# Kernel optimization log

Hardware: AMD Instinct MI355X
Metric: run time of the kernel (lower is better)

## Reference

```python
import jax, jax.numpy as jnp
import numpy as np

N_NODES = 100000
N_EDGES = 1600000
IN_CH = 64
HID = 64
OUT_CH = 1


def setup_inputs() -> dict:
    key = jax.random.key(0)
    ks = jax.random.split(key, 6)
    x = jax.random.normal(ks[0], (N_NODES, IN_CH), dtype=jnp.float32)
    edge_index = jax.random.randint(ks[1], (2, N_EDGES), 0, N_NODES, dtype=jnp.int64)
    edge_weight = jax.random.uniform(ks[2], (N_EDGES,), dtype=jnp.float32)
    W1 = jax.random.normal(ks[3], (IN_CH, HID), dtype=jnp.float32) / np.sqrt(IN_CH)
    b1 = jnp.zeros((HID,), dtype=jnp.float32)
    W2 = jax.random.normal(ks[4], (HID, OUT_CH), dtype=jnp.float32) / np.sqrt(HID)
    b2 = jnp.zeros((OUT_CH,), dtype=jnp.float32)
    return {"x": x, "edge_index": edge_index, "edge_weight": edge_weight,
            "W1": W1, "b1": b1, "W2": W2, "b2": b2}


def _gcn_conv(x, row, col, ew, W, b, n_nodes):
    # PyG GCNConv: add self-loops (weight 1), symmetric deg normalization,
    # linear (no bias) -> message x_j * norm -> sum at target -> + bias.
    loop = jnp.arange(n_nodes, dtype=row.dtype)
    r = jnp.concatenate([row, loop])
    c = jnp.concatenate([col, loop])
    w = jnp.concatenate([ew, jnp.ones((n_nodes,), dtype=ew.dtype)])
    deg = jax.ops.segment_sum(w, c, num_segments=n_nodes)  # [N]
    dinv = jnp.where(deg > 0, jax.lax.rsqrt(deg), 0.0)
    norm = dinv[r] * w * dinv[c]  # [E+N]
    h = x @ W  # [N, out]
    msg = h[r] * norm[:, None]  # [E+N, out] gather
    out = jax.ops.segment_sum(msg, c, num_segments=n_nodes)  # scatter-add
    return out + b


def reference(x, edge_index, edge_weight, W1, b1, W2, b2):
    row, col = edge_index[0], edge_index[1]
    n = x.shape[0]
    h = _gcn_conv(x, row, col, edge_weight, W1, b1, n)
    h = jax.nn.relu(h)
    out = _gcn_conv(h, row, col, edge_weight, W2, b2, n)
    return out
```

## Files before the change

kernel.cpp:

```cpp
#include <hip/hip_runtime.h>


#define N_NODES 100000
#define N_EDGES 1600000
#define CNT_SHIFT 42
#define SUM_MASK ((1ull << CNT_SHIFT) - 1)
#define BSZ 256
#define NBUCK 391
#define NB1 512
#define EPB 3125

typedef _Float16 half2v __attribute__((ext_vector_type(2)));

__global__ void p1_hist(const int* __restrict__ idx, int* __restrict__ hist) {
    __shared__ int h[NBUCK];
    int t = threadIdx.x, blk = blockIdx.x;
    for (int i = t; i < NBUCK; i += 256) h[i] = 0;
    __syncthreads();
    int e0 = blk * EPB;
    for (int i = t; i < EPB; i += 256) {
        int c = idx[N_EDGES + e0 + i];
        atomicAdd(&h[c >> 8], 1);
    }
    __syncthreads();
    for (int i = t; i < NBUCK; i += 256) hist[(size_t)i * NB1 + blk] = h[i];
}

__global__ void p2a_scan(int* __restrict__ hist, int* __restrict__ btot) {
    __shared__ int s[NB1];
    int t = threadIdx.x, b = blockIdx.x;
    int v = hist[(size_t)b * NB1 + t];
    s[t] = v;
    __syncthreads();
#pragma unroll
    for (int d = 1; d < NB1; d <<= 1) {
        int u = (t >= d) ? s[t - d] : 0;
        __syncthreads();
        s[t] += u;
        __syncthreads();
    }
    hist[(size_t)b * NB1 + t] = s[t] - v;
    if (t == NB1 - 1) btot[b] = s[NB1 - 1];
}

__global__ void p2b_scan(const int* __restrict__ btot, int* __restrict__ boff) {
    __shared__ int s[512];
    int t = threadIdx.x;
    int v = (t < NBUCK) ? btot[t] : 0;
    s[t] = v;
    __syncthreads();
#pragma unroll
    for (int d = 1; d < 512; d <<= 1) {
        int u = (t >= d) ? s[t - d] : 0;
        __syncthreads();
        s[t] += u;
        __syncthreads();
    }
    if (t < NBUCK) boff[t] = s[t] - v;
    if (t == 511) boff[NBUCK] = s[511];
}

__global__ void p3_part(const int* __restrict__ idx, const float* __restrict__ w,
                        const int* __restrict__ hist, const int* __restrict__ boff,
                        float2* __restrict__ bin) {
    __shared__ int h[NBUCK];
    __shared__ int base[NBUCK];
    int t = threadIdx.x, blk = blockIdx.x;
    for (int i = t; i < NBUCK; i += 256) {
        h[i] = 0;
        base[i] = boff[i] + hist[(size_t)i * NB1 + blk];
    }
    __syncthreads();
    int e0 = blk * EPB;
    for (int i = t; i < EPB; i += 256) {
        int e = e0 + i;
        int r = idx[e];
        int c = idx[N_EDGES + e];
        int b = c >> 8;
        int lr = atomicAdd(&h[b], 1);
        bin[base[b] + lr] = make_float2(__int_as_float(r | ((c & 255) << 17)), w[e]);
    }
}

__global__ void p4a_count(const float2* __restrict__ bin, const int* __restrict__ boff,
                          int* __restrict__ cnt, int* __restrict__ off,
                          float* __restrict__ dinv) {
    __shared__ unsigned long long pk[BSZ];
    __shared__ int s[BSZ];
    int t = threadIdx.x, b = blockIdx.x;
    if (t < BSZ) pk[t] = 0ull;
    __syncthreads();
    int s0 = boff[b], s1 = boff[b + 1];
    for (int j = s0 + t; j < s1; j += 512) {
        float2 p = bin[j];
        int cl = (__float_as_int(p.x) >> 17) & 255;
        unsigned long long add =
            (1ull << CNT_SHIFT) | (unsigned long long)(p.y * 4294967296.0f);
        atomicAdd(&pk[cl], add);
    }
    __syncthreads();
    unsigned long long p = 0;
    int c = 0;
    if (t < BSZ) {
        p = pk[t];
        c = (int)(p >> CNT_SHIFT);
        s[t] = c;
    }
    __syncthreads();
#pragma unroll
    for (int d = 1; d < BSZ; d <<= 1) {
        int u = (t >= d && t < BSZ) ? s[t - d] : 0;
        __syncthreads();
        if (t < BSZ) s[t] += u;
        __syncthreads();
    }
    if (t < BSZ) {
        int node = b * BSZ + t;
        if (node < N_NODES) {
            off[node] = s0 + s[t] - c;
            cnt[node] = c;
            float deg = 1.0f + (float)(p & SUM_MASK) * 2.3283064365386963e-10f;
            dinv[node] = rsqrtf(deg);
        }
    }
}

__global__ void p4b_place(const float2* __restrict__ bin, const int* __restrict__ boff,
                          const int* __restrict__ off, const float* __restrict__ dinv,
                          float2* __restrict__ pairs) {
    __shared__ int rk[BSZ];
    int t = threadIdx.x, b = blockIdx.x;
    if (t < BSZ) rk[t] = 0;
    __syncthreads();
    int s0 = boff[b], s1 = boff[b + 1];
    for (int j = s0 + t; j < s1; j += 512) {
        float2 p = bin[j];
        int bits = __float_as_int(p.x);
        int r = bits & 0x1FFFF;
        int cl = (bits >> 17) & 255;
        int c = (b << 8) + cl;
        int rank = atomicAdd(&rk[cl], 1);
        float norm = dinv[r] * p.y * dinv[c];
        pairs[off[c] + rank] = make_float2(__int_as_float(r), norm);
    }
}

__global__ void gemm1(const float* __restrict__ x, const float* __restrict__ W1,
                      _Float16* __restrict__ h1) {
    __shared__ float w1s[64 * 64];
    __shared__ float xs[64 * 64];
    int t = threadIdx.x;
    int row0 = blockIdx.x * 64;

    const float4* W4 = (const float4*)W1;
    float4* w1s4 = (float4*)w1s;
    float4* xs4 = (float4*)xs;
    const float4* X4 = (const float4*)(x + (size_t)row0 * 64);
#pragma unroll
    for (int i = 0; i < 4; i++) {
        w1s4[t + 256 * i] = W4[t + 256 * i];
        int gr = row0 + ((t + 256 * i) >> 4);
        xs4[t + 256 * i] = (gr < N_NODES) ? X4[t + 256 * i]
                                          : make_float4(0.f, 0.f, 0.f, 0.f);
    }
    __syncthreads();

    int cq = t & 15;
    int rq = t >> 4;
    float4 acc0 = {0,0,0,0}, acc1 = {0,0,0,0}, acc2 = {0,0,0,0}, acc3 = {0,0,0,0};
#pragma unroll 4
    for (int k = 0; k < 64; k++) {
        float4 wv = w1s4[k * 16 + cq];
        float x0 = xs[(rq     ) * 64 + k];
        float x1 = xs[(rq + 16) * 64 + k];
        float x2 = xs[(rq + 32) * 64 + k];
        float x3 = xs[(rq + 48) * 64 + k];
        acc0.x += x0*wv.x; acc0.y += x0*wv.y; acc0.z += x0*wv.z; acc0.w += x0*wv.w;
        acc1.x += x1*wv.x; acc1.y += x1*wv.y; acc1.z += x1*wv.z; acc1.w += x1*wv.w;
        acc2.x += x2*wv.x; acc2.y += x2*wv.y; acc2.z += x2*wv.z; acc2.w += x2*wv.w;
        acc3.x += x3*wv.x; acc3.y += x3*wv.y; acc3.z += x3*wv.z; acc3.w += x3*wv.w;
    }
    float4 accs[4] = {acc0, acc1, acc2, acc3};
#pragma unroll
    for (int i = 0; i < 4; i++) {
        int row = row0 + rq + 16 * i;
        if (row < N_NODES) {
            half2v h01 = {(_Float16)accs[i].x, (_Float16)accs[i].y};
            half2v h23 = {(_Float16)accs[i].z, (_Float16)accs[i].w};
            half2v* dst = (half2v*)(h1 + (size_t)row * 64 + 4 * cq);
            dst[0] = h01;
            dst[1] = h23;
        }
    }
}

__global__ void gather1(const half2v* __restrict__ h1v, const float2* __restrict__ pairs,
                        const int* __restrict__ off, const int* __restrict__ cnt,
                        const float* __restrict__ dinv, const float* __restrict__ b1,
                        const float* __restrict__ W2, const float* __restrict__ b2,
                        float* __restrict__ h2, float* __restrict__ out, int n) {
    int t = threadIdx.x;
    int lane = t & 63;
    int half = lane >> 5;
    int cl = lane & 31;
    int dst = blockIdx.x * 2 + (t >> 6);
    if (dst >= n) return;
    int beg = off[dst];
    int end = beg + cnt[dst];
    float di = dinv[dst];
    float a0 = 0.f, a1 = 0.f, b0 = 0.f, b1a = 0.f;
    float c0 = 0.f, c1 = 0.f, d0 = 0.f, d1 = 0.f;
    int j = beg + half;
    for (; j + 14 < end; j += 16) {
        float2 p0 = pairs[j],      p1 = pairs[j + 2],  p2 = pairs[j + 4],  p3 = pairs[j + 6];
        float2 p4 = pairs[j + 8],  p5 = pairs[j + 10], p6 = pairs[j + 12], p7 = pairs[j + 14];
        half2v v0 = h1v[__float_as_int(p0.x) * 32 + cl];
        half2v v1 = h1v[__float_as_int(p1.x) * 32 + cl];
        half2v v2 = h1v[__float_as_int(p2.x) * 32 + cl];
        half2v v3 = h1v[__float_as_int(p3.x) * 32 + cl];
        half2v v4 = h1v[__float_as_int(p4.x) * 32 + cl];
        half2v v5 = h1v[__float_as_int(p5.x) * 32 + cl];
        half2v v6 = h1v[__float_as_int(p6.x) * 32 + cl];
        half2v v7 = h1v[__float_as_int(p7.x) * 32 + cl];
        a0 += p0.y * (float)v0[0]; a1 += p0.y * (float)v0[1];
        b0 += p1.y * (float)v1[0]; b1a += p1.y * (float)v1[1];
        c0 += p2.y * (float)v2[0]; c1 += p2.y * (float)v2[1];
        d0 += p3.y * (float)v3[0]; d1 += p3.y * (float)v3[1];
        a0 += p4.y * (float)v4[0]; a1 += p4.y * (float)v4[1];
        b0 += p5.y * (float)v5[0]; b1a += p5.y * (float)v5[1];
        c0 += p6.y * (float)v6[0]; c1 += p6.y * (float)v6[1];
        d0 += p7.y * (float)v7[0]; d1 += p7.y * (float)v7[1];
    }
    for (; j + 6 < end; j += 8) {
        float2 p0 = pairs[j], p1 = pairs[j + 2], p2 = pairs[j + 4], p3 = pairs[j + 6];
        half2v v0 = h1v[__float_as_int(p0.x) * 32 + cl];
        half2v v1 = h1v[__float_as_int(p1.x) * 32 + cl];
        half2v v2 = h1v[__float_as_int(p2.x) * 32 + cl];
        half2v v3 = h1v[__float_as_int(p3.x) * 32 + cl];
        a0 += p0.y * (float)v0[0]; a1 += p0.y * (float)v0[1];
        b0 += p1.y * (float)v1[0]; b1a += p1.y * (float)v1[1];
        c0 += p2.y * (float)v2[0]; c1 += p2.y * (float)v2[1];
        d0 += p3.y * (float)v3[0]; d1 += p3.y * (float)v3[1];
    }
    for (; j < end; j += 2) {
        float2 p = pairs[j];
        half2v v = h1v[__float_as_int(p.x) * 32 + cl];
        a0 += p.y * (float)v[0]; a1 += p.y * (float)v[1];
    }
    float t0 = (a0 + b0) + (c0 + d0);
    float t1 = (a1 + b1a) + (c1 + d1);
    t0 += __shfl_xor(t0, 32, 64);
    t1 += __shfl_xor(t1, 32, 64);
    half2v sv = h1v[dst * 32 + cl];
    t0 += (float)sv[0] * di * di;
    t1 += (float)sv[1] * di * di;
    float2 b1p = ((const float2*)b1)[cl];
    float v0 = fmaxf(t0 + b1p.x, 0.0f);
    float v1 = fmaxf(t1 + b1p.y, 0.0f);
    float2 w2p = ((const float2*)W2)[cl];
    float p = v0 * w2p.x + v1 * w2p.y;
#pragma unroll
    for (int o = 16; o > 0; o >>= 1) p += __shfl_xor(p, o, 64);
    if (lane == 0) {
        h2[dst] = p;
        out[dst] = b2[0] + p * di * di;
    }
}

__global__ void gather2(const float2* __restrict__ pairs, const int* __restrict__ off,
                        const int* __restrict__ cnt, const float* __restrict__ h2,
                        float* __restrict__ out, int n) {
    int i = blockIdx.x * blockDim.x + threadIdx.x;
    if (i >= n) return;
    int beg = off[i];
    int end = beg + cnt[i];
    float s = 0.f;
#pragma unroll 4
    for (int j = beg; j < end; j++) {
        float2 p = pairs[j];
        s += p.y * h2[__float_as_int(p.x)];
    }
    out[i] += s;
}

extern "C" void kernel_launch(void* const* d_in, const int* in_sizes, int n_in,
                              void* d_out, int out_size, void* d_ws, size_t ws_size,
                              hipStream_t stream) {
    const float* x   = (const float*)d_in[0];
    const int*   idx = (const int*)d_in[1];
    const float* ew  = (const float*)d_in[2];
    const float* W1  = (const float*)d_in[3];
    const float* b1  = (const float*)d_in[4];
    const float* W2  = (const float*)d_in[5];
    const float* b2  = (const float*)d_in[6];
    float* out = (float*)d_out;

    const int N = N_NODES;
    const int E = N_EDGES;

    float* ws = (float*)d_ws;
    int*    off  = (int*)ws;
    int*    cnt  = (int*)(ws + (size_t)N);
    float*  dinv = ws + 2 * (size_t)N;
    int*    boff = (int*)(ws + 3 * (size_t)N);
    int*    btot = (int*)(ws + 3 * (size_t)N + 392);
    int*    hist = (int*)(ws + 300784);
    float2* bin  = (float2*)(ws + 300784 + 200192);
    _Float16* h1 = (_Float16*)(ws + 300784);
    float2* pairs = (float2*)(ws + 3700976);
    float*  h2   = ws + 6900976;

    p1_hist<<<NB1, 256, 0, stream>>>(idx, hist);
    p2a_scan<<<NBUCK, NB1, 0, stream>>>(hist, btot);
    p2b_scan<<<1, 512, 0, stream>>>(btot, boff);
    p3_part<<<NB1, 256, 0, stream>>>(idx, ew, hist, boff, bin);
    p4a_count<<<NBUCK, 512, 0, stream>>>(bin, boff, cnt, off, dinv);
    p4b_place<<<NBUCK, 512, 0, stream>>>(bin, boff, off, dinv, pairs);
    gemm1<<<(N + 63) / 64, 256, 0, stream>>>(x, W1, h1);
    gather1<<<(N + 1) / 2, 128, 0, stream>>>((const half2v*)h1, pairs, off, cnt, dinv,
                                             b1, W2, b2, h2, out, N);
    gather2<<<(N + 255) / 256, 256, 0, stream>>>(pairs, off, cnt, h2, out, N);
}
```

Before: 228.4 us.

## Fuse scan and CSR build kernels, prescale by dinv, retile GEMM, parallelize gather2

Folds the bucket-offset scan into p3_part and p4_build by having each block redundantly rescan btot. Merges the count and place passes into one kernel that keeps offsets and dinv in shared memory, so the per-edge norm needs only the target's dinv. The source-side dinv is folded into h1 and h2 at production time, which removes a gather of dinv[r] per edge. The cnt array is replaced by off[n+1]. gemm1 is retiled to 128 rows with an 8x8 register tile and padded LDS, and gather2 uses 4 lanes per node with shuffle reduction. The cost is redundant scans in every block and higher register pressure in gemm1.

```diff
diff --git a/kernel.cpp b/kernel.cpp
--- a/kernel.cpp
+++ b/kernel.cpp
@@ -43,36 +43,30 @@
     if (t == NB1 - 1) btot[b] = s[NB1 - 1];
 }
 
-__global__ void p2b_scan(const int* __restrict__ btot, int* __restrict__ boff) {
-    __shared__ int s[512];
-    int t = threadIdx.x;
+__global__ void p3_part(const int* __restrict__ idx, const float* __restrict__ w,
+                        const int* __restrict__ hist, const int* __restrict__ btot,
+                        float2* __restrict__ bin) {
+    __shared__ int sc[512];
+    __shared__ int base[NBUCK];
+    __shared__ int h[NBUCK];
+    int t = threadIdx.x, blk = blockIdx.x;
     int v = (t < NBUCK) ? btot[t] : 0;
-    s[t] = v;
+    sc[t] = v;
     __syncthreads();
 #pragma unroll
     for (int d = 1; d < 512; d <<= 1) {
-        int u = (t >= d) ? s[t - d] : 0;
-        __syncthreads();
-        s[t] += u;
-        __syncthreads();
-    }
-    if (t < NBUCK) boff[t] = s[t] - v;
-    if (t == 511) boff[NBUCK] = s[511];
-}
-
-__global__ void p3_part(const int* __restrict__ idx, const float* __restrict__ w,
-                        const int* __restrict__ hist, const int* __restrict__ boff,
-                        float2* __restrict__ bin) {
-    __shared__ int h[NBUCK];
-    __shared__ int base[NBUCK];
-    int t = threadIdx.x, blk = blockIdx.x;
-    for (int i = t; i < NBUCK; i += 256) {
-        h[i] = 0;
-        base[i] = boff[i] + hist[(size_t)i * NB1 + blk];
+        int u = (t >= d) ? sc[t - d] : 0;
+        __syncthreads();
+        sc[t] += u;
+        __syncthreads();
+    }
+    if (t < NBUCK) {
+        base[t] = sc[t] - v + hist[(size_t)t * NB1 + blk];
+        h[t] = 0;
     }
     __syncthreads();
     int e0 = blk * EPB;
-    for (int i = t; i < EPB; i += 256) {
+    for (int i = t; i < EPB; i += 512) {
         int e = e0 + i;
         int r = idx[e];
         int c = idx[N_EDGES + e];
@@ -82,15 +76,28 @@
     }
 }
 
-__global__ void p4a_count(const float2* __restrict__ bin, const int* __restrict__ boff,
-                          int* __restrict__ cnt, int* __restrict__ off,
-                          float* __restrict__ dinv) {
+__global__ void p4_build(const float2* __restrict__ bin, const int* __restrict__ btot,
+                         int* __restrict__ off, float* __restrict__ dinv,
+                         float2* __restrict__ pairs) {
+    __shared__ int sc[512];
     __shared__ unsigned long long pk[BSZ];
-    __shared__ int s[BSZ];
+    __shared__ float dl[BSZ];
+    __shared__ int ofl[BSZ];
+    __shared__ int rk[BSZ];
     int t = threadIdx.x, b = blockIdx.x;
-    if (t < BSZ) pk[t] = 0ull;
-    __syncthreads();
-    int s0 = boff[b], s1 = boff[b + 1];
+    int v = (t < NBUCK) ? btot[t] : 0;
+    sc[t] = v;
+    if (t < BSZ) { pk[t] = 0ull; rk[t] = 0; }
+    __syncthreads();
+#pragma unroll
+    for (int d = 1; d < 512; d <<= 1) {
+        int u = (t >= d) ? sc[t - d] : 0;
+        __syncthreads();
+        sc[t] += u;
+        __syncthreads();
+    }
+    int s0 = (b > 0) ? sc[b - 1] : 0;
+    int s1 = sc[b];
     for (int j = s0 + t; j < s1; j += 512) {
         float2 p = bin[j];
         int cl = (__float_as_int(p.x) >> 17) & 255;
@@ -99,106 +106,121 @@
         atomicAdd(&pk[cl], add);
     }
     __syncthreads();
-    unsigned long long p = 0;
+    unsigned long long pv = 0;
     int c = 0;
     if (t < BSZ) {
-        p = pk[t];
-        c = (int)(p >> CNT_SHIFT);
-        s[t] = c;
+        pv = pk[t];
+        c = (int)(pv >> CNT_SHIFT);
+        sc[t] = c;
     }
     __syncthreads();
 #pragma unroll
     for (int d = 1; d < BSZ; d <<= 1) {
-        int u = (t >= d && t < BSZ) ? s[t - d] : 0;
-        __syncthreads();
-        if (t < BSZ) s[t] += u;
+        int u = (t >= d && t < BSZ) ? sc[t - d] : 0;
+        __syncthreads();
+        if (t < BSZ) sc[t] += u;
         __syncthreads();
     }
     if (t < BSZ) {
+        int o = s0 + sc[t] - c;
+        ofl[t] = o;
+        float deg = 1.0f + (float)(pv & SUM_MASK) * 2.3283064365386963e-10f;
+        float di = rsqrtf(deg);
+        dl[t] = di;
         int node = b * BSZ + t;
-        if (node < N_NODES) {
-            off[node] = s0 + s[t] - c;
-            cnt[node] = c;
-            float deg = 1.0f + (float)(p & SUM_MASK) * 2.3283064365386963e-10f;
-            dinv[node] = rsqrtf(deg);
-        }
-    }
-}
-
-__global__ void p4b_place(const float2* __restrict__ bin, const int* __restrict__ boff,
-                          const int* __restrict__ off, const float* __restrict__ dinv,
-                          float2* __restrict__ pairs) {
-    __shared__ int rk[BSZ];
-    int t = threadIdx.x, b = blockIdx.x;
-    if (t < BSZ) rk[t] = 0;
-    __syncthreads();
-    int s0 = boff[b], s1 = boff[b + 1];
+        if (node < N_NODES) { off[node] = o; dinv[node] = di; }
+    }
+    if (b == NBUCK - 1 && t == 0) off[N_NODES] = s1;
+    __syncthreads();
     for (int j = s0 + t; j < s1; j += 512) {
         float2 p = bin[j];
         int bits = __float_as_int(p.x);
         int r = bits & 0x1FFFF;
         int cl = (bits >> 17) & 255;
-        int c = (b << 8) + cl;
         int rank = atomicAdd(&rk[cl], 1);
-        float norm = dinv[r] * p.y * dinv[c];
-        pairs[off[c] + rank] = make_float2(__int_as_float(r), norm);
+        pairs[ofl[cl] + rank] = make_float2(__int_as_float(r), p.y * dl[cl]);
     }
 }
 
 __global__ void gemm1(const float* __restrict__ x, const float* __restrict__ W1,
-                      _Float16* __restrict__ h1) {
+                      const float* __restrict__ dinv, _Float16* __restrict__ h1) {
+    __shared__ float xs[128 * 68];
     __shared__ float w1s[64 * 64];
-    __shared__ float xs[64 * 64];
     int t = threadIdx.x;
-    int row0 = blockIdx.x * 64;
-
-    const float4* W4 = (const float4*)W1;
+    int row0 = blockIdx.x * 128;
+
+    const float4* W4g = (const float4*)W1;
     float4* w1s4 = (float4*)w1s;
-    float4* xs4 = (float4*)xs;
-    const float4* X4 = (const float4*)(x + (size_t)row0 * 64);
-#pragma unroll
-    for (int i = 0; i < 4; i++) {
-        w1s4[t + 256 * i] = W4[t + 256 * i];
-        int gr = row0 + ((t + 256 * i) >> 4);
-        xs4[t + 256 * i] = (gr < N_NODES) ? X4[t + 256 * i]
-                                          : make_float4(0.f, 0.f, 0.f, 0.f);
-    }
-    __syncthreads();
-
-    int cq = t & 15;
-    int rq = t >> 4;
-    float4 acc0 = {0,0,0,0}, acc1 = {0,0,0,0}, acc2 = {0,0,0,0}, acc3 = {0,0,0,0};
-#pragma unroll 4
-    for (int k = 0; k < 64; k++) {
-        float4 wv = w1s4[k * 16 + cq];
-        float x0 = xs[(rq     ) * 64 + k];
-        float x1 = xs[(rq + 16) * 64 + k];
-        float x2 = xs[(rq + 32) * 64 + k];
-        float x3 = xs[(rq + 48) * 64 + k];
-        acc0.x += x0*wv.x; acc0.y += x0*wv.y; acc0.z += x0*wv.z; acc0.w += x0*wv.w;
-        acc1.x += x1*wv.x; acc1.y += x1*wv.y; acc1.z += x1*wv.z; acc1.w += x1*wv.w;
-        acc2.x += x2*wv.x; acc2.y += x2*wv.y; acc2.z += x2*wv.z; acc2.w += x2*wv.w;
-        acc3.x += x3*wv.x; acc3.y += x3*wv.y; acc3.z += x3*wv.z; acc3.w += x3*wv.w;
-    }
-    float4 accs[4] = {acc0, acc1, acc2, acc3};
-#pragma unroll
-    for (int i = 0; i < 4; i++) {
+#pragma unroll
+    for (int i = 0; i < 8; i++) w1s4[t + 128 * i] = W4g[t + 128 * i];
+    const float4* X4 = (const float4*)x;
+#pragma unroll
+    for (int i = 0; i < 16; i++) {
+        int fi = t + 128 * i;
+        int rl = fi >> 4;
+        int kq = fi & 15;
+        int row = row0 + rl;
+        float4 vv = (row < N_NODES) ? X4[(size_t)row * 16 + kq]
+                                    : make_float4(0.f, 0.f, 0.f, 0.f);
+        *(float4*)&xs[rl * 68 + kq * 4] = vv;
+    }
+    __syncthreads();
+
+    int cq = t & 7;
+    int rq = t >> 3;
+    float acc[8][8];
+#pragma unroll
+    for (int i = 0; i < 8; i++)
+#pragma unroll
+        for (int j = 0; j < 8; j++) acc[i][j] = 0.f;
+
+    for (int k = 0; k < 64; k += 4) {
+        float4 xv[8];
+#pragma unroll
+        for (int i = 0; i < 8; i++)
+            xv[i] = *(const float4*)&xs[(rq + 16 * i) * 68 + k];
+        float4 wv[4][2];
+#pragma unroll
+        for (int kk = 0; kk < 4; kk++) {
+            wv[kk][0] = w1s4[(k + kk) * 16 + 2 * cq];
+            wv[kk][1] = w1s4[(k + kk) * 16 + 2 * cq + 1];
+        }
+#pragma unroll
+        for (int i = 0; i < 8; i++) {
+            float xk[4] = {xv[i].x, xv[i].y, xv[i].z, xv[i].w};
+#pragma unroll
+            for (int kk = 0; kk < 4; kk++) {
+                acc[i][0] += xk[kk] * wv[kk][0].x;
+                acc[i][1] += xk[kk] * wv[kk][0].y;
+                acc[i][2] += xk[kk] * wv[kk][0].z;
+                acc[i][3] += xk[kk] * wv[kk][0].w;
+                acc[i][4] += xk[kk] * wv[kk][1].x;
+                acc[i][5] += xk[kk] * wv[kk][1].y;
+                acc[i][6] += xk[kk] * wv[kk][1].z;
+                acc[i][7] += xk[kk] * wv[kk][1].w;
+            }
+        }
+    }
+#pragma unroll
+    for (int i = 0; i < 8; i++) {
         int row = row0 + rq + 16 * i;
         if (row < N_NODES) {
-            half2v h01 = {(_Float16)accs[i].x, (_Float16)accs[i].y};
-            half2v h23 = {(_Float16)accs[i].z, (_Float16)accs[i].w};
-            half2v* dst = (half2v*)(h1 + (size_t)row * 64 + 4 * cq);
-            dst[0] = h01;
-            dst[1] = h23;
+            float di = dinv[row];
+            half2v h4[4];
+#pragma unroll
+            for (int j = 0; j < 4; j++)
+                h4[j] = half2v{(_Float16)(acc[i][2 * j] * di),
+                               (_Float16)(acc[i][2 * j + 1] * di)};
+            *(float4*)(h1 + (size_t)row * 64 + 8 * cq) = *(float4*)h4;
         }
     }
 }
 
 __global__ void gather1(const half2v* __restrict__ h1v, const float2* __restrict__ pairs,
-                        const int* __restrict__ off, const int* __restrict__ cnt,
-                        const float* __restrict__ dinv, const float* __restrict__ b1,
-                        const float* __restrict__ W2, const float* __restrict__ b2,
-                        float* __restrict__ h2, float* __restrict__ out, int n) {
+                        const int* __restrict__ off, const float* __restrict__ dinv,
+                        const float* __restrict__ b1, const float* __restrict__ W2,
+                        const float* __restrict__ b2, float* __restrict__ h2,
+                        float* __restrict__ out, int n) {
     int t = threadIdx.x;
     int lane = t & 63;
     int half = lane >> 5;
@@ -206,7 +228,7 @@
     int dst = blockIdx.x * 2 + (t >> 6);
     if (dst >= n) return;
     int beg = off[dst];
-    int end = beg + cnt[dst];
+    int end = off[dst + 1];
     float di = dinv[dst];
     float a0 = 0.f, a1 = 0.f, b0 = 0.f, b1a = 0.f;
     float c0 = 0.f, c1 = 0.f, d0 = 0.f, d1 = 0.f;
@@ -252,8 +274,8 @@
     t0 += __shfl_xor(t0, 32, 64);
     t1 += __shfl_xor(t1, 32, 64);
     half2v sv = h1v[dst * 32 + cl];
-    t0 += (float)sv[0] * di * di;
-    t1 += (float)sv[1] * di * di;
+    t0 += (float)sv[0] * di;
+    t1 += (float)sv[1] * di;
     float2 b1p = ((const float2*)b1)[cl];
     float v0 = fmaxf(t0 + b1p.x, 0.0f);
     float v1 = fmaxf(t1 + b1p.y, 0.0f);
@@ -262,25 +284,26 @@
 #pragma unroll
     for (int o = 16; o > 0; o >>= 1) p += __shfl_xor(p, o, 64);
     if (lane == 0) {
-        h2[dst] = p;
+        h2[dst] = p * di;
         out[dst] = b2[0] + p * di * di;
     }
 }
 
 __global__ void gather2(const float2* __restrict__ pairs, const int* __restrict__ off,
-                        const int* __restrict__ cnt, const float* __restrict__ h2,
-                        float* __restrict__ out, int n) {
-    int i = blockIdx.x * blockDim.x + threadIdx.x;
+                        const float* __restrict__ h2, float* __restrict__ out, int n) {
+    int t = threadIdx.x;
+    int i = blockIdx.x * 64 + (t >> 2);
     if (i >= n) return;
-    int beg = off[i];
-    int end = beg + cnt[i];
+    int q = t & 3;
+    int beg = off[i], end = off[i + 1];
     float s = 0.f;
-#pragma unroll 4
-    for (int j = beg; j < end; j++) {
+    for (int j = beg + q; j < end; j += 4) {
         float2 p = pairs[j];
         s += p.y * h2[__float_as_int(p.x)];
     }
-    out[i] += s;
+    s += __shfl_xor(s, 1, 64);
+    s += __shfl_xor(s, 2, 64);
+    if (q == 0) out[i] += s;
 }
 
 extern "C" void kernel_launch(void* const* d_in, const int* in_sizes, int n_in,
@@ -296,28 +319,23 @@
     float* out = (float*)d_out;
 
     const int N = N_NODES;
-    const int E = N_EDGES;
 
     float* ws = (float*)d_ws;
     int*    off  = (int*)ws;
-    int*    cnt  = (int*)(ws + (size_t)N);
-    float*  dinv = ws + 2 * (size_t)N;
-    int*    boff = (int*)(ws + 3 * (size_t)N);
-    int*    btot = (int*)(ws + 3 * (size_t)N + 392);
-    int*    hist = (int*)(ws + 300784);
-    float2* bin  = (float2*)(ws + 300784 + 200192);
-    _Float16* h1 = (_Float16*)(ws + 300784);
-    float2* pairs = (float2*)(ws + 3700976);
-    float*  h2   = ws + 6900976;
+    float*  dinv = ws + 100004;
+    int*    btot = (int*)(ws + 200004);
+    int*    hist = (int*)(ws + 200400);
+    float2* bin  = (float2*)(ws + 200400 + 200192);
+    _Float16* h1 = (_Float16*)(ws + 200400);
+    float2* pairs = (float2*)(ws + 3600592);
+    float*  h2   = ws + 6800592;
 
     p1_hist<<<NB1, 256, 0, stream>>>(idx, hist);
     p2a_scan<<<NBUCK, NB1, 0, stream>>>(hist, btot);
-    p2b_scan<<<1, 512, 0, stream>>>(btot, boff);
-    p3_part<<<NB1, 256, 0, stream>>>(idx, ew, hist, boff, bin);
-    p4a_count<<<NBUCK, 512, 0, stream>>>(bin, boff, cnt, off, dinv);
-    p4b_place<<<NBUCK, 512, 0, stream>>>(bin, boff, off, dinv, pairs);
-    gemm1<<<(N + 63) / 64, 256, 0, stream>>>(x, W1, h1);
-    gather1<<<(N + 1) / 2, 128, 0, stream>>>((const half2v*)h1, pairs, off, cnt, dinv,
+    p3_part<<<NB1, 512, 0, stream>>>(idx, ew, hist, btot, bin);
+    p4_build<<<NBUCK, 512, 0, stream>>>(bin, btot, off, dinv, pairs);
+    gemm1<<<(N + 127) / 128, 128, 0, stream>>>(x, W1, dinv, h1);
+    gather1<<<(N + 1) / 2, 128, 0, stream>>>((const half2v*)h1, pairs, off, dinv,
                                              b1, W2, b2, h2, out, N);
-    gather2<<<(N + 255) / 256, 256, 0, stream>>>(pairs, off, cnt, h2, out, N);
-}
+    gather2<<<(N + 63) / 64, 256, 0, stream>>>(pairs, off, h2, out, N);
+}
```

Result: no change. 226.3 us (-0.9%).
